# Kernel optimization log

Hardware: AMD Instinct MI355X
Metric: run time of the kernel (lower is better)

The kernel has to match this reference:

```python
import jax, jax.numpy as jnp
import numpy as np

COMMITMENT_COST = 0.25


def setup_inputs() -> dict:
    key = jax.random.key(0)
    k1, k2 = jax.random.split(key)
    inputs = jax.random.normal(k1, (16, 1024, 256), dtype=jnp.float32)
    embeddings = jax.random.normal(k2, (8192, 256), dtype=jnp.float32) * 0.1
    return {"inputs": inputs, "embeddings": embeddings}


def reference(inputs, embeddings):
    K, D = embeddings.shape
    input_shape = inputs.shape
    flat = inputs.reshape(-1, D)  # [N, D]
    distances = (
        jnp.sum(flat * flat, axis=1, keepdims=True)
        + jnp.sum(embeddings * embeddings, axis=1)
        - 2.0 * jnp.matmul(flat, embeddings.T)
    )
    encoding_indices = jnp.argmin(distances, axis=1)  # [N]
    # direct codebook gather (same math as one-hot @ embeddings)
    quantized = embeddings[encoding_indices].reshape(input_shape)
    quantized_sg = inputs + jax.lax.stop_gradient(quantized - inputs)
    e_latent_loss = jnp.mean((jax.lax.stop_gradient(quantized) - inputs) ** 2)
    q_latent_loss = jnp.mean((quantized_sg - jax.lax.stop_gradient(quantized)) ** 2)
    loss = q_latent_loss + COMMITMENT_COST * e_latent_loss
    # avg one-hot probabilities = normalized codeword counts
    N = flat.shape[0]
    counts = jnp.zeros((K,), dtype=flat.dtype).at[encoding_indices].add(1.0)
    avg_probs = counts / N
    perplexity = jnp.exp(-jnp.sum(avg_probs * jnp.log(avg_probs + 1e-10)))
    return quantized_sg, encoding_indices, loss, perplexity
```

## Files before the change

### kernel.cpp

```cpp
#include <hip/hip_runtime.h>
#include <math.h>
#include <stdint.h>

#define ND_ROWS 16384
#define DDIM    256
#define KCODES  8192
#define NSEG    128
#define NRG     8

typedef _Float16 f16x4 __attribute__((ext_vector_type(4)));
typedef _Float16 f16x8 __attribute__((ext_vector_type(8)));
typedef float    f32x4v __attribute__((ext_vector_type(4)));
typedef float    f32x16 __attribute__((ext_vector_type(16)));


__device__ __attribute__((always_inline)) inline void load_lds16(const void* g, void* l) {
    __builtin_amdgcn_global_load_lds((const __attribute__((address_space(1))) void*)g,
                                     (__attribute__((address_space(3))) void*)l, 16, 0, 0);
}

__global__ __launch_bounds__(256) void prep_kernel(const float* __restrict__ x,
                                                   const float* __restrict__ emb,
                                                   _Float16* __restrict__ Xp,
                                                   _Float16* __restrict__ Bp,
                                                   float* __restrict__ neF,
                                                   unsigned long long* __restrict__ minpair,
                                                   int* __restrict__ counts) {
    __shared__ __align__(16) _Float16 S[16384];
    const int bid = blockIdx.x;
    const int tid = threadIdx.x;

    if (bid < 512) {
        const int rb = bid;
        const float4* src = (const float4*)(x + (size_t)rb * 32 * DDIM);
        #pragma unroll
        for (int i = 0; i < 8; ++i) {
            int g = i * 256 + tid;
            float4 v = src[g];
            int rl = g >> 6;
            int k0 = (g & 63) << 2;
            f16x4 hi, lo;
            hi[0] = (_Float16)v.x; lo[0] = (_Float16)(v.x - (float)hi[0]);
            hi[1] = (_Float16)v.y; lo[1] = (_Float16)(v.y - (float)hi[1]);
            hi[2] = (_Float16)v.z; lo[2] = (_Float16)(v.z - (float)hi[2]);
            hi[3] = (_Float16)v.w; lo[3] = (_Float16)(v.w - (float)hi[3]);
            int off = ((k0 >> 4) << 9) + (((k0 >> 3) & 1) << 8)
                    + (rl << 3) + (((k0 >> 2) & 1) << 2);
            *(f16x4*)(S + off)        = hi;
            *(f16x4*)(S + off + 8192) = lo;
        }
        if (tid < 32) minpair[rb * 32 + tid] = 0xFFFFFFFFFFFFFFFFull;
        __syncthreads();
        float4* dst = (float4*)(Xp + (size_t)rb * 16384);
        const float4* sls = (const float4*)S;
        #pragma unroll
        for (int i = 0; i < 8; ++i) {
            int g = i * 256 + tid;
            dst[g] = sls[g];
        }
    } else {
        int wave = ((bid - 512) << 2) + (tid >> 6);
        int lane = tid & 63;
        int r    = wave;
        const float* src = emb + (size_t)r * DDIM;
        float4 v = ((const float4*)src)[lane];
        float s = v.x*v.x + v.y*v.y + v.z*v.z + v.w*v.w;
        #pragma unroll
        for (int m = 32; m; m >>= 1) s += __shfl_xor(s, m, 64);
        float4 t;
        t.x = -2.0f * v.x; t.y = -2.0f * v.y; t.z = -2.0f * v.z; t.w = -2.0f * v.w;
        f16x4 hi, lo;
        hi[0] = (_Float16)t.x; lo[0] = (_Float16)(t.x - (float)hi[0]);
        hi[1] = (_Float16)t.y; lo[1] = (_Float16)(t.y - (float)hi[1]);
        hi[2] = (_Float16)t.z; lo[2] = (_Float16)(t.z - (float)hi[2]);
        hi[3] = (_Float16)t.w; lo[3] = (_Float16)(t.w - (float)hi[3]);
        _Float16* dst = Bp + (size_t)r * 512;
        *(f16x4*)(dst + lane * 4)       = hi;
        *(f16x4*)(dst + 256 + lane * 4) = lo;
        if (lane == 0) {
            neF[r] = s;
            counts[r] = 0;
        }
    }
}

#define MFMA16(A, B, C) __builtin_amdgcn_mfma_f32_32x32x16_f16(A, B, C, 0, 0, 0)

__global__ __launch_bounds__(512, 4) void argmin_seg(
    const _Float16* __restrict__ Xp, const _Float16* __restrict__ Bp,
    const float* __restrict__ neF, unsigned long long* __restrict__ minpair) {
    __shared__ __align__(16) _Float16 Cs[64 * 512];

    const int tid  = threadIdx.x;
    const int lane = tid & 63;
    const int w    = tid >> 6;
    const int c32  = lane & 31;
    const int kg   = lane >> 5;

    const int rg      = blockIdx.x & 7;
    const int seg     = blockIdx.x >> 3;
    const int rowBase = rg * 2048;
    const int code0   = seg * 64;

    #pragma unroll
    for (int i = 0; i < 8; ++i) {
        int j    = w * 8 + i;
        int code = code0 + (j & 32) + (lane & 31);
        int s    = ((j & 31) << 1) | (lane >> 5);
        load_lds16((const char*)Bp + ((size_t)code << 10) + (s << 4),
                   (char*)Cs + (j << 10));
    }
    __syncthreads();

    const char* cpb = (const char*)Cs + (kg << 9) + (c32 << 4);

    const int wBase = rowBase + w * 256;
    for (int c2 = 0; c2 < 4; ++c2) {
        const int rb0 = (wBase >> 5) + c2 * 2;
        const char* xb0 = (const char*)Xp + (size_t)rb0 * 32768 + lane * 16;
        const char* xb1 = xb0 + 32768;
        f32x16 acc[2][2];
        #pragma unroll
        for (int i = 0; i < 16; ++i) {
            acc[0][0][i] = 0.0f; acc[0][1][i] = 0.0f;
            acc[1][0][i] = 0.0f; acc[1][1][i] = 0.0f;
        }

        #pragma unroll 2
        for (int q = 0; q < 16; ++q) {
            f16x8 xh0 = *(const f16x8*)(xb0 + q * 1024);
            f16x8 xl0 = *(const f16x8*)(xb0 + 16384 + q * 1024);
            f16x8 xh1 = *(const f16x8*)(xb1 + q * 1024);
            f16x8 xl1 = *(const f16x8*)(xb1 + 16384 + q * 1024);
            f16x8 ch0 = *(const f16x8*)(cpb + q * 1024);
            f16x8 cl0 = *(const f16x8*)(cpb + 16384 + q * 1024);
            f16x8 ch1 = *(const f16x8*)(cpb + 32768 + q * 1024);
            f16x8 cl1 = *(const f16x8*)(cpb + 49152 + q * 1024);
            acc[0][0] = MFMA16(ch0, xh0, acc[0][0]);
            acc[0][1] = MFMA16(ch1, xh0, acc[0][1]);
            acc[1][0] = MFMA16(ch0, xh1, acc[1][0]);
            acc[1][1] = MFMA16(ch1, xh1, acc[1][1]);
            acc[0][0] = MFMA16(ch0, xl0, acc[0][0]);
            acc[0][1] = MFMA16(ch1, xl0, acc[0][1]);
            acc[1][0] = MFMA16(ch0, xl1, acc[1][0]);
            acc[1][1] = MFMA16(ch1, xl1, acc[1][1]);
            acc[0][0] = MFMA16(cl0, xh0, acc[0][0]);
            acc[0][1] = MFMA16(cl1, xh0, acc[0][1]);
            acc[1][0] = MFMA16(cl0, xh1, acc[1][0]);
            acc[1][1] = MFMA16(cl1, xh1, acc[1][1]);
        }

        f32x4v ne4[2][4];
        #pragma unroll
        for (int mt = 0; mt < 2; ++mt)
            #pragma unroll
            for (int g2 = 0; g2 < 4; ++g2)
                ne4[mt][g2] = *(const f32x4v*)(neF + code0 + mt * 32 + g2 * 8 + 4 * kg);
        #pragma unroll
        for (int ck = 0; ck < 2; ++ck) {
            float best = 3.402823466e+38f;
            int   bi   = 0;
            #pragma unroll
            for (int mt = 0; mt < 2; ++mt)
                #pragma unroll
                for (int r = 0; r < 16; ++r) {
                    float d  = acc[ck][mt][r] + ne4[mt][r >> 2][r & 3];
                    int   id = code0 + mt * 32 + 4 * kg + ((r & 3) + 8 * (r >> 2));
                    if (d < best) { best = d; bi = id; }
                }
            float ov = __shfl_xor(best, 32, 64);
            int   oi = __shfl_xor(bi, 32, 64);
            if (ov < best || (ov == best && oi < bi)) { best = ov; bi = oi; }
            if (kg == 0) {
                int row = (rb0 + ck) * 32 + c32;
                unsigned u = __float_as_uint(best);
                u = (u & 0x80000000u) ? ~u : (u | 0x80000000u);
                atomicMin(&minpair[row],
                          (((unsigned long long)u) << 32) | (unsigned)bi);
            }
        }
    }
}

__global__ __launch_bounds__(256) void finalize_kernel(
    const float* __restrict__ x, const float* __restrict__ emb,
    const unsigned long long* __restrict__ minpair,
    float* __restrict__ out_q, float* __restrict__ out_idx,
    int* __restrict__ counts, float* __restrict__ parts) {
    __shared__ float rde[4], rdq[4];
    int wv   = threadIdx.x >> 6;
    int row  = (blockIdx.x << 2) + wv;
    int lane = threadIdx.x & 63;

    int bi = (int)(minpair[row] & 0xFFFFFFFFull);

    float4 xv = ((const float4*)(x   + (size_t)row * DDIM))[lane];
    float4 ev = ((const float4*)(emb + (size_t)bi  * DDIM))[lane];
    float4 q;
    q.x = xv.x + (ev.x - xv.x);
    q.y = xv.y + (ev.y - xv.y);
    q.z = xv.z + (ev.z - xv.z);
    q.w = xv.w + (ev.w - xv.w);
    ((float4*)(out_q + (size_t)row * DDIM))[lane] = q;

    float de = (ev.x - xv.x) * (ev.x - xv.x) + (ev.y - xv.y) * (ev.y - xv.y)
             + (ev.z - xv.z) * (ev.z - xv.z) + (ev.w - xv.w) * (ev.w - xv.w);
    float dq = (q.x - ev.x) * (q.x - ev.x) + (q.y - ev.y) * (q.y - ev.y)
             + (q.z - ev.z) * (q.z - ev.z) + (q.w - ev.w) * (q.w - ev.w);
    #pragma unroll
    for (int m = 32; m; m >>= 1) {
        de += __shfl_xor(de, m, 64);
        dq += __shfl_xor(dq, m, 64);
    }
    if (lane == 0) {
        out_idx[row] = (float)bi;
        atomicAdd(&counts[bi], 1);
        rde[wv] = de; rdq[wv] = dq;
    }
    __syncthreads();
    if (threadIdx.x == 0) {
        parts[blockIdx.x]        = rde[0] + rde[1] + rde[2] + rde[3];
        parts[4096 + blockIdx.x] = rdq[0] + rdq[1] + rdq[2] + rdq[3];
    }
}

__global__ __launch_bounds__(256) void scalars_kernel(
    const int* __restrict__ counts, const float* __restrict__ parts,
    float* __restrict__ out_loss, float* __restrict__ out_perp) {
    __shared__ float red[256], rde[256], rdq[256];
    float local = 0.0f, de = 0.0f, dq = 0.0f;
    for (int k = threadIdx.x; k < KCODES; k += 256) {
        float p = (float)counts[k] * (1.0f / (float)ND_ROWS);
        local += p * logf(p + 1e-10f);
    }
    for (int k = threadIdx.x; k < 4096; k += 256) {
        de += parts[k];
        dq += parts[4096 + k];
    }
    red[threadIdx.x] = local; rde[threadIdx.x] = de; rdq[threadIdx.x] = dq;
    __syncthreads();
    for (int s = 128; s; s >>= 1) {
        if (threadIdx.x < s) {
            red[threadIdx.x] += red[threadIdx.x + s];
            rde[threadIdx.x] += rde[threadIdx.x + s];
            rdq[threadIdx.x] += rdq[threadIdx.x + s];
        }
        __syncthreads();
    }
    if (threadIdx.x == 0) {
        *out_perp = expf(-red[0]);
        float invn = 1.0f / (float)(ND_ROWS * DDIM);
        *out_loss = rdq[0] * invn + 0.25f * (rde[0] * invn);
    }
}

extern "C" void kernel_launch(void* const* d_in, const int* in_sizes, int n_in,
                              void* d_out, int out_size, void* d_ws, size_t ws_size,
                              hipStream_t stream) {
    const float* x   = (const float*)d_in[0];
    const float* emb = (const float*)d_in[1];

    char* ws = (char*)d_ws;
    unsigned long long* minpair = (unsigned long long*)ws;
    int*      counts = (int*)(ws + 131072);
    float*    parts  = (float*)(ws + 163840);
    float*    neF    = (float*)(ws + 196608);
    _Float16* Xp     = (_Float16*)(ws + 229376);
    _Float16* Bp     = (_Float16*)(ws + 17006592);

    float* out_q    = (float*)d_out;
    float* out_idx  = out_q + (size_t)ND_ROWS * DDIM;
    float* out_loss = out_idx + ND_ROWS;
    float* out_perp = out_loss + 1;

    prep_kernel<<<512 + KCODES / 4, 256, 0, stream>>>(x, emb, Xp, Bp, neF,
                                                      minpair, counts);
    argmin_seg<<<NRG * NSEG, 512, 0, stream>>>(Xp, Bp, neF, minpair);
    finalize_kernel<<<ND_ROWS / 4, 256, 0, stream>>>(x, emb, minpair,
                                                     out_q, out_idx, counts, parts);
    scalars_kernel<<<1, 256, 0, stream>>>(counts, parts, out_loss, out_perp);
}
```

Baseline: 307.7 us.

## Switch argmin kernel to 16x16x32 MFMA with 32-code segments

Restructures the distance/argmin kernel to use 16x16x32 f16 MFMA tiles. Each block now holds 32 codes instead of 64, so LDS per block is halved and the launch bound allows 8 blocks per CU. The grid doubles to 2048 blocks and each wave processes 8 row blocks of 32 rows with far fewer accumulator registers. The aim is higher occupancy and lower register pressure. The cost is that X tiles are re-read from global memory twice as often, and there are more atomicMin operations plus an extra cross-lane reduction step.

```diff
diff --git a/kernel.cpp b/kernel.cpp
--- a/kernel.cpp
+++ b/kernel.cpp
@@ -5,7 +5,7 @@
 #define ND_ROWS 16384
 #define DDIM    256
 #define KCODES  8192
-#define NSEG    128
+#define NSEG16  256
 #define NRG     8
 
 typedef _Float16 f16x4 __attribute__((ext_vector_type(4)));
@@ -84,95 +84,102 @@
     }
 }
 
-#define MFMA16(A, B, C) __builtin_amdgcn_mfma_f32_32x32x16_f16(A, B, C, 0, 0, 0)
-
-__global__ __launch_bounds__(512, 4) void argmin_seg(
+#define MFMA16x16(A, B, C) __builtin_amdgcn_mfma_f32_16x16x32_f16(A, B, C, 0, 0, 0)
+
+__global__ __launch_bounds__(512, 8) void argmin_seg(
     const _Float16* __restrict__ Xp, const _Float16* __restrict__ Bp,
     const float* __restrict__ neF, unsigned long long* __restrict__ minpair) {
-    __shared__ __align__(16) _Float16 Cs[64 * 512];
+    __shared__ __align__(16) _Float16 Cs[16384];
 
     const int tid  = threadIdx.x;
     const int lane = tid & 63;
     const int w    = tid >> 6;
-    const int c32  = lane & 31;
-    const int kg   = lane >> 5;
+    const int c16  = lane & 15;
+    const int l4   = lane >> 4;
 
     const int rg      = blockIdx.x & 7;
     const int seg     = blockIdx.x >> 3;
     const int rowBase = rg * 2048;
-    const int code0   = seg * 64;
+    const int code0   = seg * 32;
 
     #pragma unroll
-    for (int i = 0; i < 8; ++i) {
-        int j    = w * 8 + i;
-        int code = code0 + (j & 32) + (lane & 31);
-        int s    = ((j & 31) << 1) | (lane >> 5);
-        load_lds16((const char*)Bp + ((size_t)code << 10) + (s << 4),
+    for (int i = 0; i < 4; ++i) {
+        int j    = w * 4 + i;
+        int code = code0 + ((j >> 4) << 4) + c16;
+        int oct  = ((j & 15) << 2) | l4;
+        load_lds16((const char*)Bp + ((size_t)code << 10) + (oct << 4),
                    (char*)Cs + (j << 10));
     }
     __syncthreads();
 
-    const char* cpb = (const char*)Cs + (kg << 9) + (c32 << 4);
-
-    const int wBase = rowBase + w * 256;
-    for (int c2 = 0; c2 < 4; ++c2) {
-        const int rb0 = (wBase >> 5) + c2 * 2;
-        const char* xb0 = (const char*)Xp + (size_t)rb0 * 32768 + lane * 16;
-        const char* xb1 = xb0 + 32768;
-        f32x16 acc[2][2];
-        #pragma unroll
-        for (int i = 0; i < 16; ++i) {
-            acc[0][0][i] = 0.0f; acc[0][1][i] = 0.0f;
-            acc[1][0][i] = 0.0f; acc[1][1][i] = 0.0f;
-        }
+    const char* ca = (const char*)Cs + (lane << 4);
+    const int rbBase = (rowBase >> 5) + w * 8;
+
+    #pragma unroll 1
+    for (int p = 0; p < 8; ++p) {
+        const int rb = rbBase + p;
+        const char* xb = (const char*)Xp + (size_t)rb * 32768
+                       + (l4 << 9) + (c16 << 4);
+
+        f32x4v a00, a01, a10, a11;
+        #pragma unroll
+        for (int i = 0; i < 4; ++i) { a00[i] = 0.0f; a01[i] = 0.0f;
+                                      a10[i] = 0.0f; a11[i] = 0.0f; }
 
         #pragma unroll 2
-        for (int q = 0; q < 16; ++q) {
-            f16x8 xh0 = *(const f16x8*)(xb0 + q * 1024);
-            f16x8 xl0 = *(const f16x8*)(xb0 + 16384 + q * 1024);
-            f16x8 xh1 = *(const f16x8*)(xb1 + q * 1024);
-            f16x8 xl1 = *(const f16x8*)(xb1 + 16384 + q * 1024);
-            f16x8 ch0 = *(const f16x8*)(cpb + q * 1024);
-            f16x8 cl0 = *(const f16x8*)(cpb + 16384 + q * 1024);
-            f16x8 ch1 = *(const f16x8*)(cpb + 32768 + q * 1024);
-            f16x8 cl1 = *(const f16x8*)(cpb + 49152 + q * 1024);
-            acc[0][0] = MFMA16(ch0, xh0, acc[0][0]);
-            acc[0][1] = MFMA16(ch1, xh0, acc[0][1]);
-            acc[1][0] = MFMA16(ch0, xh1, acc[1][0]);
-            acc[1][1] = MFMA16(ch1, xh1, acc[1][1]);
-            acc[0][0] = MFMA16(ch0, xl0, acc[0][0]);
-            acc[0][1] = MFMA16(ch1, xl0, acc[0][1]);
-            acc[1][0] = MFMA16(ch0, xl1, acc[1][0]);
-            acc[1][1] = MFMA16(ch1, xl1, acc[1][1]);
-            acc[0][0] = MFMA16(cl0, xh0, acc[0][0]);
-            acc[0][1] = MFMA16(cl1, xh0, acc[0][1]);
-            acc[1][0] = MFMA16(cl0, xh1, acc[1][0]);
-            acc[1][1] = MFMA16(cl1, xh1, acc[1][1]);
-        }
-
-        f32x4v ne4[2][4];
-        #pragma unroll
-        for (int mt = 0; mt < 2; ++mt)
-            #pragma unroll
-            for (int g2 = 0; g2 < 4; ++g2)
-                ne4[mt][g2] = *(const f32x4v*)(neF + code0 + mt * 32 + g2 * 8 + 4 * kg);
-        #pragma unroll
-        for (int ck = 0; ck < 2; ++ck) {
+        for (int t = 0; t < 8; ++t) {
+            f16x8 xh0 = *(const f16x8*)(xb + t * 2048);
+            f16x8 xh1 = *(const f16x8*)(xb + t * 2048 + 256);
+            f16x8 xl0 = *(const f16x8*)(xb + 16384 + t * 2048);
+            f16x8 xl1 = *(const f16x8*)(xb + 16384 + t * 2048 + 256);
+            f16x8 ch0 = *(const f16x8*)(ca + t * 1024);
+            f16x8 ch1 = *(const f16x8*)(ca + 16384 + t * 1024);
+            a00 = MFMA16x16(ch0, xh0, a00);
+            a01 = MFMA16x16(ch1, xh0, a01);
+            a10 = MFMA16x16(ch0, xh1, a10);
+            a11 = MFMA16x16(ch1, xh1, a11);
+            a00 = MFMA16x16(ch0, xl0, a00);
+            a01 = MFMA16x16(ch1, xl0, a01);
+            a10 = MFMA16x16(ch0, xl1, a10);
+            a11 = MFMA16x16(ch1, xl1, a11);
+            f16x8 cl0 = *(const f16x8*)(ca + 8192 + t * 1024);
+            f16x8 cl1 = *(const f16x8*)(ca + 24576 + t * 1024);
+            a00 = MFMA16x16(cl0, xh0, a00);
+            a01 = MFMA16x16(cl1, xh0, a01);
+            a10 = MFMA16x16(cl0, xh1, a10);
+            a11 = MFMA16x16(cl1, xh1, a11);
+        }
+
+        __builtin_amdgcn_sched_barrier(0);
+
+        f32x4v ne0 = *(const f32x4v*)(neF + code0 + (l4 << 2));
+        f32x4v ne1 = *(const f32x4v*)(neF + code0 + 16 + (l4 << 2));
+        #pragma unroll
+        for (int rt = 0; rt < 2; ++rt) {
+            f32x4v d0 = rt ? a10 : a00;
+            f32x4v d1 = rt ? a11 : a01;
             float best = 3.402823466e+38f;
             int   bi   = 0;
             #pragma unroll
-            for (int mt = 0; mt < 2; ++mt)
-                #pragma unroll
-                for (int r = 0; r < 16; ++r) {
-                    float d  = acc[ck][mt][r] + ne4[mt][r >> 2][r & 3];
-                    int   id = code0 + mt * 32 + 4 * kg + ((r & 3) + 8 * (r >> 2));
-                    if (d < best) { best = d; bi = id; }
-                }
-            float ov = __shfl_xor(best, 32, 64);
-            int   oi = __shfl_xor(bi, 32, 64);
+            for (int r = 0; r < 4; ++r) {
+                float d  = d0[r] + ne0[r];
+                int   id = code0 + (l4 << 2) + r;
+                if (d < best) { best = d; bi = id; }
+            }
+            #pragma unroll
+            for (int r = 0; r < 4; ++r) {
+                float d  = d1[r] + ne1[r];
+                int   id = code0 + 16 + (l4 << 2) + r;
+                if (d < best) { best = d; bi = id; }
+            }
+            float ov = __shfl_xor(best, 16, 64);
+            int   oi = __shfl_xor(bi, 16, 64);
             if (ov < best || (ov == best && oi < bi)) { best = ov; bi = oi; }
-            if (kg == 0) {
-                int row = (rb0 + ck) * 32 + c32;
+            ov = __shfl_xor(best, 32, 64);
+            oi = __shfl_xor(bi, 32, 64);
+            if (ov < best || (ov == best && oi < bi)) { best = ov; bi = oi; }
+            if (lane < 16) {
+                int row = rb * 32 + rt * 16 + c16;
                 unsigned u = __float_as_uint(best);
                 u = (u & 0x80000000u) ? ~u : (u | 0x80000000u);
                 atomicMin(&minpair[row],
@@ -275,7 +282,7 @@
 
     prep_kernel<<<512 + KCODES / 4, 256, 0, stream>>>(x, emb, Xp, Bp, neF,
                                                       minpair, counts);
-    argmin_seg<<<NRG * NSEG, 512, 0, stream>>>(Xp, Bp, neF, minpair);
+    argmin_seg<<<NRG * NSEG16, 512, 0, stream>>>(Xp, Bp, neF, minpair);
     finalize_kernel<<<ND_ROWS / 4, 256, 0, stream>>>(x, emb, minpair,
                                                      out_q, out_idx, counts, parts);
     scalars_kernel<<<1, 256, 0, stream>>>(counts, parts, out_loss, out_perp);
```

Measured after the change: 314.1 us. +2.1%, slower.
